# Performance work log

Measured on AMD Instinct MI355X. Metric: run time of the kernel, lower is better.

Reference implementation:

```python
import jax, jax.numpy as jnp
import numpy as np

IM_FE_RATIO = 16.0

# 5x5 gaussian kernel from the original module (kernel_size=5)
_GK5 = np.array([[1, 4, 7, 4, 1],
                 [4, 16, 26, 16, 4],
                 [7, 26, 41, 26, 7],
                 [4, 16, 26, 16, 4],
                 [1, 4, 7, 4, 1]], dtype=np.float32) / 273.0


def setup_inputs() -> dict:
    key = jax.random.key(0)
    k1, k2, k3 = jax.random.split(key, 3)
    B, N, H, W = 16, 32, 256, 256
    # Xg: binary assignment matrix (one-hot rows), some rows zeroed (invalid matches)
    idx = jax.random.randint(k1, (B, N), 0, N)
    Xg = jax.nn.one_hot(idx, N, dtype=jnp.float32)
    valid = (jax.random.uniform(k3, (B, N, 1)) > 0.1).astype(jnp.float32)
    Xg = Xg * valid
    # keypoints in image coordinates, spanning the full feature grid after /im_fe_ratio
    keypoint_g = jax.random.uniform(k2, (B, N, 2), jnp.float32) * (W * IM_FE_RATIO - 1.0)
    gk = jnp.broadcast_to(jnp.asarray(_GK5)[None, None], (N, 1, 5, 5))  # depthwise OIHW
    return {"Xg": Xg, "keypoint_g": keypoint_g, "gk": gk, "H": H, "W": W}


def _gauss_blur(x, gk):
    # x: (B, N, H, W); depthwise 5x5 conv, zero padding (SAME)
    N = x.shape[1]
    return jax.lax.conv_general_dilated(
        x, gk, window_strides=(1, 1), padding=((2, 2), (2, 2)),
        dimension_numbers=("NCHW", "OIHW", "NCHW"), feature_group_count=N)


def reference(Xg, keypoint_g, gk, H, W):
    """InverInterpolator.forward with mode=1 (returns onehot1 from get_4nn)."""
    B, N, _ = keypoint_g.shape
    # gather ground-truth keypoint per row, convert to feature-grid coords
    xy = jnp.einsum("bij,bjk->bik", Xg, keypoint_g) / IM_FE_RATIO - 0.5  # (B,N,2)
    max_xy = jnp.array([W - 1, H - 1], jnp.float32)
    lo = jnp.clip(jnp.floor(xy), 0.0, max_xy)   # iLower (bounded)
    hi = jnp.clip(jnp.ceil(xy), 0.0, max_xy)    # iUpper (bounded)
    up = xy - lo
    lw = 1.0 - up
    ix = jnp.stack([lo[..., 0], hi[..., 0]], axis=-1)  # (B,N,2)
    iy = jnp.stack([lo[..., 1], hi[..., 1]], axis=-1)
    wx = jnp.stack([lw[..., 0], up[..., 0]], axis=-1)
    wy = jnp.stack([lw[..., 1], up[..., 1]], axis=-1)
    # 4 corners, ordered (y0x0, y0x1, y1x0, y1x1) matching the torch view
    idx4 = (iy[..., :, None] * W + ix[..., None, :]).reshape(B, N, 4).astype(jnp.int32)
    coef4 = (wy[..., :, None] * wx[..., None, :]).reshape(B, N, 4)
    # scatter 4 bilinear weights per (b,n) row into a dense HW buffer
    rows = B * N
    onehot0 = jnp.zeros((rows, H * W), jnp.float32)
    onehot0 = onehot0.at[jnp.arange(rows)[:, None], idx4.reshape(rows, 4)].add(
        coef4.reshape(rows, 4)).reshape(B, N, H * W)
    mask = jnp.sum(Xg, axis=2, keepdims=True)  # (B,N,1), validity of each row
    onehot0 = onehot0 * mask
    onehot1 = _gauss_blur(onehot0.reshape(B, N, H, W), gk).reshape(B, N, H * W)
    onehot1 = onehot1 * mask
    return onehot1
```

## Files before the change

kernel.cpp:

```cpp
#include <hip/hip_runtime.h>

__global__ __launch_bounds__(64) void patch_k(const float* __restrict__ Xg,
                                              const float* __restrict__ kp,
                                              const float* __restrict__ gk,
                                              const int* __restrict__ pH,
                                              const int* __restrict__ pW,
                                              float* __restrict__ out,
                                              int N) {
    const int H = *pH, W = *pW;
    const int bn = blockIdx.x;
    const int b  = bn / N;
    const int t  = threadIdx.x;

    const float* xrow = Xg + (size_t)bn * N;
    const float* kpb  = kp + (size_t)b * N * 2;

    float m = 0.f, sx = 0.f, sy = 0.f;
    for (int j = t; j < N; j += 64) {
        float w = xrow[j];
        m  += w;
        sx = fmaf(w, kpb[2 * j],     sx);
        sy = fmaf(w, kpb[2 * j + 1], sy);
    }
    #pragma unroll
    for (int off = 32; off > 0; off >>= 1) {
        m  += __shfl_xor(m,  off, 64);
        sx += __shfl_xor(sx, off, 64);
        sy += __shfl_xor(sy, off, 64);
    }
    if (m == 0.f) return;

    const float xf = sx * 0.0625f - 0.5f;
    const float yf = sy * 0.0625f - 0.5f;
    const float maxx = (float)(W - 1), maxy = (float)(H - 1);

    const float x0 = fminf(fmaxf(floorf(xf), 0.f), maxx);
    const float x1 = fminf(fmaxf(ceilf (xf), 0.f), maxx);
    const float y0 = fminf(fmaxf(floorf(yf), 0.f), maxy);
    const float y1 = fminf(fmaxf(ceilf (yf), 0.f), maxy);

    const float upx = xf - x0, lwx = 1.f - upx;
    const float upy = yf - y0, lwy = 1.f - upy;

    const int   xc[2] = { (int)x0, (int)x1 };
    const int   yc[2] = { (int)y0, (int)y1 };
    const float wx[2] = { lwx, upx };
    const float wy[2] = { lwy, upy };

    if (t >= 36) return;

    const int r = yc[0] - 2 + t / 6;
    const int c = xc[0] - 2 + t % 6;
    if (r < 0 || r >= H || c < 0 || c >= W) return;

    float v = 0.f;
    #pragma unroll
    for (int cy = 0; cy < 2; ++cy) {
        const int dy = yc[cy] - r + 2;
        if (dy < 0 || dy > 4) continue;
        #pragma unroll
        for (int cx = 0; cx < 2; ++cx) {
            const int dx = xc[cx] - c + 2;
            if (dx < 0 || dx > 4) continue;
            v = fmaf(wy[cy] * wx[cx], gk[dy * 5 + dx], v);
        }
    }
    out[(size_t)bn * H * W + (size_t)r * W + c] = m * m * v;
}

extern "C" void kernel_launch(void* const* d_in, const int* in_sizes, int n_in,
                              void* d_out, int out_size, void* d_ws, size_t ws_size,
                              hipStream_t stream) {
    const float* Xg = (const float*)d_in[0];
    const float* kp = (const float*)d_in[1];
    const float* gk = (const float*)d_in[2];
    const int*   pH = (const int*)d_in[3];
    const int*   pW = (const int*)d_in[4];
    float* out = (float*)d_out;

    const int BN = in_sizes[1] / 2;
    const int N  = in_sizes[0] / BN;

    hipMemsetAsync(out, 0, (size_t)out_size * sizeof(float), stream);

    patch_k<<<BN, 64, 0, stream>>>(Xg, kp, gk, pH, pW, out, N);
}
```

Measured before the change: 142.5 us.

## Fuse zero-fill and patch write into one vectorized full-output kernel

Replaces the separate memset and sparse patch kernel with a single kernel. Each block first computes the row's blurred 6x6 patch into shared memory, then writes its slice of the output plane with float4 stores: zeros outside the patch rows and patch values inside. This removes the extra launch and the memset pass. The cost is that every block redundantly recomputes the per-row keypoint reduction and waits on a block barrier.

```diff
diff --git a/kernel.cpp b/kernel.cpp
--- a/kernel.cpp
+++ b/kernel.cpp
@@ -1,71 +1,116 @@
 #include <hip/hip_runtime.h>
 
-__global__ __launch_bounds__(64) void patch_k(const float* __restrict__ Xg,
-                                              const float* __restrict__ kp,
-                                              const float* __restrict__ gk,
-                                              const int* __restrict__ pH,
-                                              const int* __restrict__ pW,
-                                              float* __restrict__ out,
-                                              int N) {
+#define TPB 256
+#define F4_PER_THREAD 8
+#define F4_PER_BLOCK (TPB * F4_PER_THREAD)
+
+__global__ __launch_bounds__(TPB) void fused_k(const float* __restrict__ Xg,
+                                               const float* __restrict__ kp,
+                                               const float* __restrict__ gk,
+                                               const int* __restrict__ pH,
+                                               const int* __restrict__ pW,
+                                               float4* __restrict__ out4,
+                                               int N) {
     const int H = *pH, W = *pW;
-    const int bn = blockIdx.x;
-    const int b  = bn / N;
+    const int W4 = W >> 2;
+    const int HW4 = H * W4;
+    const int bn = blockIdx.y;
     const int t  = threadIdx.x;
 
-    const float* xrow = Xg + (size_t)bn * N;
-    const float* kpb  = kp + (size_t)b * N * 2;
+    __shared__ float s_pv[36];
+    __shared__ int s_lo, s_hi, s_r0, s_c0;
 
-    float m = 0.f, sx = 0.f, sy = 0.f;
-    for (int j = t; j < N; j += 64) {
-        float w = xrow[j];
-        m  += w;
-        sx = fmaf(w, kpb[2 * j],     sx);
-        sy = fmaf(w, kpb[2 * j + 1], sy);
-    }
-    #pragma unroll
-    for (int off = 32; off > 0; off >>= 1) {
-        m  += __shfl_xor(m,  off, 64);
-        sx += __shfl_xor(sx, off, 64);
-        sy += __shfl_xor(sy, off, 64);
-    }
-    if (m == 0.f) return;
+    if (t < 64) {
+        const int b = bn / N;
+        const float* xrow = Xg + (size_t)bn * N;
+        const float* kpb  = kp + (size_t)b * N * 2;
 
-    const float xf = sx * 0.0625f - 0.5f;
-    const float yf = sy * 0.0625f - 0.5f;
-    const float maxx = (float)(W - 1), maxy = (float)(H - 1);
+        float m = 0.f, sx = 0.f, sy = 0.f;
+        for (int j = t; j < N; j += 64) {
+            float w = xrow[j];
+            m  += w;
+            sx = fmaf(w, kpb[2 * j],     sx);
+            sy = fmaf(w, kpb[2 * j + 1], sy);
+        }
+        #pragma unroll
+        for (int off = 32; off > 0; off >>= 1) {
+            m  += __shfl_xor(m,  off, 64);
+            sx += __shfl_xor(sx, off, 64);
+            sy += __shfl_xor(sy, off, 64);
+        }
 
-    const float x0 = fminf(fmaxf(floorf(xf), 0.f), maxx);
-    const float x1 = fminf(fmaxf(ceilf (xf), 0.f), maxx);
-    const float y0 = fminf(fmaxf(floorf(yf), 0.f), maxy);
-    const float y1 = fminf(fmaxf(ceilf (yf), 0.f), maxy);
+        if (m == 0.f) {
+            if (t == 0) { s_lo = 0; s_hi = 0; s_r0 = 0; s_c0 = 0; }
+        } else {
+            const float xf = sx * 0.0625f - 0.5f;
+            const float yf = sy * 0.0625f - 0.5f;
+            const float maxx = (float)(W - 1), maxy = (float)(H - 1);
 
-    const float upx = xf - x0, lwx = 1.f - upx;
-    const float upy = yf - y0, lwy = 1.f - upy;
+            const float x0 = fminf(fmaxf(floorf(xf), 0.f), maxx);
+            const float x1 = fminf(fmaxf(ceilf (xf), 0.f), maxx);
+            const float y0 = fminf(fmaxf(floorf(yf), 0.f), maxy);
+            const float y1 = fminf(fmaxf(ceilf (yf), 0.f), maxy);
 
-    const int   xc[2] = { (int)x0, (int)x1 };
-    const int   yc[2] = { (int)y0, (int)y1 };
-    const float wx[2] = { lwx, upx };
-    const float wy[2] = { lwy, upy };
+            const float upx = xf - x0, lwx = 1.f - upx;
+            const float upy = yf - y0, lwy = 1.f - upy;
 
-    if (t >= 36) return;
+            const int   xc[2] = { (int)x0, (int)x1 };
+            const int   yc[2] = { (int)y0, (int)y1 };
+            const float wx[2] = { lwx, upx };
+            const float wy[2] = { lwy, upy };
 
-    const int r = yc[0] - 2 + t / 6;
-    const int c = xc[0] - 2 + t % 6;
-    if (r < 0 || r >= H || c < 0 || c >= W) return;
-
-    float v = 0.f;
-    #pragma unroll
-    for (int cy = 0; cy < 2; ++cy) {
-        const int dy = yc[cy] - r + 2;
-        if (dy < 0 || dy > 4) continue;
-        #pragma unroll
-        for (int cx = 0; cx < 2; ++cx) {
-            const int dx = xc[cx] - c + 2;
-            if (dx < 0 || dx > 4) continue;
-            v = fmaf(wy[cy] * wx[cx], gk[dy * 5 + dx], v);
+            const int r0 = yc[0] - 2, c0 = xc[0] - 2;
+            if (t == 0) {
+                s_r0 = r0; s_c0 = c0;
+                s_lo = max(r0, 0) * W4;
+                s_hi = min(r0 + 6, H) * W4;
+            }
+            if (t < 36) {
+                const int rr = r0 + t / 6;
+                const int cc = c0 + t % 6;
+                float v = 0.f;
+                #pragma unroll
+                for (int cy = 0; cy < 2; ++cy) {
+                    const int dy = yc[cy] - rr + 2;
+                    if (dy < 0 || dy > 4) continue;
+                    #pragma unroll
+                    for (int cx = 0; cx < 2; ++cx) {
+                        const int dx = xc[cx] - cc + 2;
+                        if (dx < 0 || dx > 4) continue;
+                        v = fmaf(wy[cy] * wx[cx], gk[dy * 5 + dx], v);
+                    }
+                }
+                s_pv[t] = m * m * v;
+            }
         }
     }
-    out[(size_t)bn * H * W + (size_t)r * W + c] = m * m * v;
+    __syncthreads();
+
+    const int lo = s_lo, hi = s_hi, r0 = s_r0, c0 = s_c0;
+    const size_t planeBase = (size_t)bn * (size_t)HW4;
+    const int base = blockIdx.x * F4_PER_BLOCK + t;
+    const float4 z = make_float4(0.f, 0.f, 0.f, 0.f);
+
+    #pragma unroll
+    for (int k = 0; k < F4_PER_THREAD; ++k) {
+        const int L = base + k * TPB;
+        if (L >= HW4) break;
+        if (L < lo || L >= hi) {
+            out4[planeBase + L] = z;
+        } else {
+            const int row = L / W4;
+            const int colBase = (L - row * W4) << 2;
+            float4 v;
+            float* vp = (float*)&v;
+            const int dr = row - r0;
+            #pragma unroll
+            for (int j = 0; j < 4; ++j) {
+                const int dc = colBase + j - c0;
+                vp[j] = ((unsigned)dc <= 5u) ? s_pv[dr * 6 + dc] : 0.f;
+            }
+            out4[planeBase + L] = v;
+        }
+    }
 }
 
 extern "C" void kernel_launch(void* const* d_in, const int* in_sizes, int n_in,
@@ -76,12 +121,13 @@
     const float* gk = (const float*)d_in[2];
     const int*   pH = (const int*)d_in[3];
     const int*   pW = (const int*)d_in[4];
-    float* out = (float*)d_out;
+    float4* out4 = (float4*)d_out;
 
     const int BN = in_sizes[1] / 2;
     const int N  = in_sizes[0] / BN;
 
-    hipMemsetAsync(out, 0, (size_t)out_size * sizeof(float), stream);
+    const int HW4 = (out_size / BN) / 4;
+    const int chunks = (HW4 + F4_PER_BLOCK - 1) / F4_PER_BLOCK;
 
-    patch_k<<<BN, 64, 0, stream>>>(Xg, kp, gk, pH, pW, out, N);
+    fused_k<<<dim3(chunks, BN), TPB, 0, stream>>>(Xg, kp, gk, pH, pW, out4, N);
 }
```

Measured after the change: 142.5 us. Within noise of the previous version (+0.0%).
